# Kernel optimization log

Hardware: AMD Instinct MI355X
Metric: run time of the kernel (lower is better)

The kernel has to match this reference:

```python
import jax, jax.numpy as jnp
import numpy as np

B, NS, D, NE = 4096, 64, 256, 16  # walkers, determinant slots, d_model, electrons


def setup_inputs() -> dict:
    key = jax.random.key(0)
    k_y, k_up, k_dn, k_r = jax.random.split(key, 4)
    y = jax.random.normal(k_y, (B, NS, D), dtype=jnp.float32)
    # xavier_uniform over (d_model, Ne) fan axes
    limit = np.sqrt(6.0 / (D + NE)).astype(np.float32)
    M1_up_real = jax.random.uniform(k_up, (NS, D, NE), dtype=jnp.float32, minval=-limit, maxval=limit)
    M1_down_real = jax.random.uniform(k_dn, (NS, D, NE), dtype=jnp.float32, minval=-limit, maxval=limit)
    # R: Ne distinct orbital-row indices per walker in [0, 2*Ns)
    keys = jax.random.split(k_r, B)
    R = jax.vmap(lambda k: jax.random.permutation(k, 2 * NS)[:NE])(keys).astype(jnp.int32)
    return {"y": y, "M1_up_real": M1_up_real, "M1_down_real": M1_down_real, "R": R}


def reference(y, M1_up_real, M1_down_real, R):
    # orbitals: per-slot linear map of features -> Ne orbital values
    orb_up = jnp.einsum('bnd,nde->bne', y, M1_up_real)      # (B, Ns, Ne)
    orb_dn = jnp.einsum('bnd,nde->bne', y, M1_down_real)    # (B, Ns, Ne)
    orbitals = jnp.concatenate((orb_up, orb_dn), axis=1)     # (B, 2*Ns, Ne)
    # gather Ne rows per walker -> batched square matrices (B, Ne, Ne)
    A = jnp.take_along_axis(orbitals, R[:, :, None], axis=1)
    sign, logabsdet = jnp.linalg.slogdet(A)
    cdtype = jnp.complex64
    amp = logabsdet.astype(cdtype) + jnp.log(sign.astype(cdtype))
    return jnp.where(jnp.isnan(amp), -jnp.inf, amp)          # (B,) complex64
```

## Files before the change

kernel.cpp:

```cpp
#include <hip/hip_runtime.h>
#include <math.h>

#define BWALK 4096
#define NS 64
#define DD 256
#define NE 16
#define NSLOT 128
#define CHUNK 512
#define ROWB 528

typedef __attribute__((ext_vector_type(4))) float f32x4;
typedef __attribute__((ext_vector_type(8))) short s16x8;

union Frag  { s16x8 v; unsigned u[4]; uint4 q; };

__device__ inline unsigned rne_bf16(float x) {
    unsigned u = __float_as_uint(x);
    return (u + 0x7fffu + ((u >> 16) & 1u)) >> 16;
}
__device__ inline float bf16_to_f(unsigned h) { return __uint_as_float(h << 16); }

__global__ __launch_bounds__(256) void convert_m_kernel(
    const float* __restrict__ Mup,
    const float* __restrict__ Mdn,
    uint4* __restrict__ Mhi,
    uint4* __restrict__ Mlo)
{
    const int t = blockIdx.x * 256 + threadIdx.x;
    const int n    = t >> 9;
    const int kc   = (t >> 6) & 7;
    const int lane = t & 63;
    const int kg = lane >> 4;
    const int e  = lane & 15;

    const float* Msrc = (n < NS ? Mup : Mdn) + (size_t)(n & (NS - 1)) * (DD * NE);

    unsigned h[8], l[8];
    #pragma unroll
    for (int j = 0; j < 8; ++j) {
        const int k = kc * 32 + kg * 8 + j;
        const float f = Msrc[k * 16 + e];
        const unsigned hh = rne_bf16(f);
        h[j] = hh;
        l[j] = rne_bf16(f - bf16_to_f(hh));
    }
    uint4 vh, vl;
    vh.x = h[0] | (h[1] << 16); vh.y = h[2] | (h[3] << 16);
    vh.z = h[4] | (h[5] << 16); vh.w = h[6] | (h[7] << 16);
    vl.x = l[0] | (l[1] << 16); vl.y = l[2] | (l[3] << 16);
    vl.z = l[4] | (l[5] << 16); vl.w = l[6] | (l[7] << 16);
    Mhi[t] = vh;
    Mlo[t] = vl;
}

__global__ __launch_bounds__(256) void orbitals_kernel(
    const float* __restrict__ y,
    const int* __restrict__ R,
    const uint4* __restrict__ Mhi,
    const uint4* __restrict__ Mlo,
    float* __restrict__ A)
{
    const int n   = blockIdx.x;
    const int b0  = blockIdx.y * CHUNK;
    const int tid = threadIdx.x;
    const int lane = tid & 63;
    const int wv   = tid >> 6;

    __shared__ __align__(16) unsigned char sY[4 * 2 * 16 * ROWB];
    __shared__ int sCode[CHUNK];
    __shared__ int wsum[4];

    int m[2];
    int cnt = 0;
    #pragma unroll
    for (int q = 0; q < 2; ++q) {
        const int b = b0 + tid * 2 + q;
        const int4* rp = (const int4*)(R + (size_t)b * NE);
        int mi = -1;
        #pragma unroll
        for (int t4 = 0; t4 < 4; ++t4) {
            const int4 r4 = rp[t4];
            if (r4.x == n) mi = t4 * 4 + 0;
            if (r4.y == n) mi = t4 * 4 + 1;
            if (r4.z == n) mi = t4 * 4 + 2;
            if (r4.w == n) mi = t4 * 4 + 3;
        }
        m[q] = mi;
        cnt += (mi >= 0) ? 1 : 0;
    }

    int incl = cnt;
    #pragma unroll
    for (int off = 1; off < 64; off <<= 1) {
        const int x = __shfl_up(incl, off, 64);
        if (lane >= off) incl += x;
    }
    if (lane == 63) wsum[wv] = incl;
    __syncthreads();
    int base = incl - cnt;
    #pragma unroll
    for (int w = 0; w < 3; ++w) if (w < wv) base += wsum[w];
    const int total = wsum[0] + wsum[1] + wsum[2] + wsum[3];
    {
        int p = base;
        #pragma unroll
        for (int q = 0; q < 2; ++q) {
            if (m[q] >= 0) {
                const int b = b0 + tid * 2 + q;
                sCode[p++] = (b << 4) | m[q];
            }
        }
    }
    __syncthreads();

    if (total == 0) return;

    const int e  = lane & 15;
    const int kg = lane >> 4;
    const int slot = n & (NS - 1);
    const uint4* bhp = Mhi + ((size_t)n * 8) * 64 + lane;
    const uint4* blp = Mlo + ((size_t)n * 8) * 64 + lane;

    char* waveBase = (char*)sY + wv * (2 * 16 * ROWB);
    char* hiBase = waveBase;
    char* loBase = waveBase + 16 * ROWB;

    for (int g = wv * 16; g < total; g += 64) {
        Frag BH[8], BL[8];
        #pragma unroll
        for (int kc = 0; kc < 8; ++kc) {
            BH[kc].q = bhp[kc * 64];
            BL[kc].q = blp[kc * 64];
        }

        f32x4 vv[16];
        #pragma unroll
        for (int r = 0; r < 16; ++r) {
            const int idx = g + r;
            const int code = sCode[idx < total ? idx : (total - 1)];
            const float* row = y + ((size_t)(code >> 4) * NS + slot) * DD;
            vv[r] = ((const f32x4*)row)[lane];
        }
        #pragma unroll
        for (int r = 0; r < 16; ++r) {
            unsigned h[4], l[4];
            #pragma unroll
            for (int j = 0; j < 4; ++j) {
                const float f = vv[r][j];
                h[j] = rne_bf16(f);
                l[j] = rne_bf16(f - bf16_to_f(h[j]));
            }
            uint2 hw, lw;
            hw.x = h[0] | (h[1] << 16); hw.y = h[2] | (h[3] << 16);
            lw.x = l[0] | (l[1] << 16); lw.y = l[2] | (l[3] << 16);
            *(uint2*)(hiBase + r * ROWB + lane * 8) = hw;
            *(uint2*)(loBase + r * ROWB + lane * 8) = lw;
        }

        const int gme = g + e;
        const int mycode = sCode[gme < total ? gme : (total - 1)];

        f32x4 acc0 = {0.f, 0.f, 0.f, 0.f};
        f32x4 acc1 = {0.f, 0.f, 0.f, 0.f};
        f32x4 acc2 = {0.f, 0.f, 0.f, 0.f};
        #pragma unroll
        for (int kc = 0; kc < 8; ++kc) {
            Frag ahi, alo;
            ahi.q = *(const uint4*)(hiBase + e * ROWB + kg * 16 + kc * 64);
            alo.q = *(const uint4*)(loBase + e * ROWB + kg * 16 + kc * 64);
            acc0 = __builtin_amdgcn_mfma_f32_16x16x32_bf16(ahi.v, BH[kc].v, acc0, 0, 0, 0);
            acc1 = __builtin_amdgcn_mfma_f32_16x16x32_bf16(ahi.v, BL[kc].v, acc1, 0, 0, 0);
            acc2 = __builtin_amdgcn_mfma_f32_16x16x32_bf16(alo.v, BH[kc].v, acc2, 0, 0, 0);
        }
        const f32x4 acc = acc0 + (acc1 + acc2);

        #pragma unroll
        for (int r = 0; r < 4; ++r) {
            const int j = kg * 4 + r;
            const int jcode = __shfl(mycode, j, 16);
            if (g + j < total) A[(size_t)jcode * NE + e] = acc[r];
        }
    }
}

__global__ __launch_bounds__(256) void lu_det_kernel(
    const float* __restrict__ A, float* __restrict__ out, int mode)
{
    const int tid = threadIdx.x;
    const int w = blockIdx.x * 16 + (tid >> 4);
    const int lane = tid & 15;

    float a[NE];
    {
        const f32x4* p = (const f32x4*)(A + ((size_t)w * NE + lane) * NE);
        #pragma unroll
        for (int q = 0; q < 4; ++q) {
            const f32x4 vv = p[q];
            a[q * 4 + 0] = vv[0]; a[q * 4 + 1] = vv[1];
            a[q * 4 + 2] = vv[2]; a[q * 4 + 3] = vv[3];
        }
    }

    unsigned used = 0u;
    float logabs = 0.0f;
    int neg = 0;
    int perm[NE];

    #pragma unroll
    for (int k = 0; k < NE; ++k) {
        float v = ((used >> lane) & 1u) ? -1.0f : fabsf(a[k]);
        int bi = lane;
        #pragma unroll
        for (int off = 8; off > 0; off >>= 1) {
            const float ov = __shfl_xor(v, off, 16);
            const int   oi = __shfl_xor(bi, off, 16);
            if (ov > v || (ov == v && oi < bi)) { v = ov; bi = oi; }
        }
        const int p = bi;
        perm[k] = p;
        const float pivval = __shfl(a[k], p, 16);
        const bool active = (((used >> lane) & 1u) == 0u) && (lane != p);
        const float mlt = active ? (a[k] / pivval) : 0.0f;
        #pragma unroll
        for (int ee = k + 1; ee < NE; ++ee) {
            const float pe = __shfl(a[ee], p, 16);
            a[ee] = fmaf(-mlt, pe, a[ee]);
        }
        used |= (1u << p);
        logabs += logf(fabsf(pivval));
        neg ^= (pivval < 0.0f) ? 1 : 0;
    }

    int inv = 0;
    #pragma unroll
    for (int k1 = 0; k1 < NE; ++k1) {
        #pragma unroll
        for (int k2 = k1 + 1; k2 < NE; ++k2)
            inv ^= (perm[k1] > perm[k2]) ? 1 : 0;
    }
    neg ^= inv;

    if (lane == 0) {
        float re = logabs;
        float im = neg ? 3.14159274101257324f : 0.0f;
        if (__builtin_isnan(re)) { re = -INFINITY; im = 0.0f; }
        else if (re == -INFINITY) { im = 0.0f; }
        if (mode == 0) { out[2 * w] = re; out[2 * w + 1] = im; }
        else           { out[w] = re; }
    }
}

__global__ __launch_bounds__(256) void outputheaddet_kernel(
    const float* __restrict__ y,
    const float* __restrict__ Mup,
    const float* __restrict__ Mdn,
    const int* __restrict__ R,
    float* __restrict__ out,
    int mode)
{
    const int b = blockIdx.x;
    const int tid = threadIdx.x;

    __shared__ int   sR[NE];
    __shared__ float sYf[NE][DD];
    __shared__ float sA[NE][NE + 1];

    if (tid < NE) sR[tid] = R[b * NE + tid];
    __syncthreads();

    {
        const int i  = tid >> 4;
        const int d0 = (tid & 15) * 16;
        const int n    = sR[i];
        const int slot = n & (NS - 1);
        const float4* yp = reinterpret_cast<const float4*>(
            y + (((size_t)b * NS + slot) * DD + d0));
        float4 v0 = yp[0], v1 = yp[1], v2 = yp[2], v3 = yp[3];
        float4* dst = reinterpret_cast<float4*>(&sYf[i][d0]);
        dst[0] = v0; dst[1] = v1; dst[2] = v2; dst[3] = v3;
    }
    __syncthreads();

    {
        const int i = tid >> 4;
        const int e = tid & 15;
        const int n    = sR[i];
        const int slot = n & (NS - 1);
        const float* Mp = (n < NS ? Mup : Mdn) + (size_t)slot * (DD * NE) + e;
        float acc = 0.0f;
        #pragma unroll 8
        for (int d = 0; d < DD; ++d)
            acc = fmaf(sYf[i][d], Mp[(size_t)d * NE], acc);
        sA[i][e] = acc;
    }
    __syncthreads();

    if (tid >= NE) return;

    const int lane = tid;
    float a[NE];
    #pragma unroll
    for (int e = 0; e < NE; ++e) a[e] = sA[lane][e];

    unsigned used = 0u;
    float logabs = 0.0f;
    int neg = 0;
    int perm[NE];

    #pragma unroll
    for (int k = 0; k < NE; ++k) {
        float v = ((used >> lane) & 1u) ? -1.0f : fabsf(a[k]);
        int bi = lane;
        #pragma unroll
        for (int off = 8; off > 0; off >>= 1) {
            float ov = __shfl_xor(v, off, 16);
            int   oi = __shfl_xor(bi, off, 16);
            if (ov > v || (ov == v && oi < bi)) { v = ov; bi = oi; }
        }
        const int p = bi;
        perm[k] = p;
        const float pivval = __shfl(a[k], p, 16);
        const bool active = (((used >> lane) & 1u) == 0u) && (lane != p);
        const float mlt = active ? (a[k] / pivval) : 0.0f;
        #pragma unroll
        for (int e = k + 1; e < NE; ++e) {
            const float pe = __shfl(a[e], p, 16);
            a[e] = fmaf(-mlt, pe, a[e]);
        }
        used |= (1u << p);
        logabs += logf(fabsf(pivval));
        neg ^= (pivval < 0.0f) ? 1 : 0;
    }

    int inv = 0;
    #pragma unroll
    for (int k1 = 0; k1 < NE; ++k1) {
        #pragma unroll
        for (int k2 = k1 + 1; k2 < NE; ++k2)
            inv ^= (perm[k1] > perm[k2]) ? 1 : 0;
    }
    neg ^= inv;

    if (lane == 0) {
        float re = logabs;
        float im = neg ? 3.14159274101257324f : 0.0f;
        if (__builtin_isnan(re)) { re = -INFINITY; im = 0.0f; }
        else if (re == -INFINITY) { im = 0.0f; }
        if (mode == 0) { out[2 * b] = re; out[2 * b + 1] = im; }
        else           { out[b] = re; }
    }
}

extern "C" void kernel_launch(void* const* d_in, const int* in_sizes, int n_in,
                              void* d_out, int out_size, void* d_ws, size_t ws_size,
                              hipStream_t stream) {
    const float* y   = (const float*)d_in[0];
    const float* Mup = (const float*)d_in[1];
    const float* Mdn = (const float*)d_in[2];
    const int*   R   = (const int*)d_in[3];
    float* out = (float*)d_out;

    const int mode = (out_size >= 2 * BWALK) ? 0 : 1;

    const size_t frag_bytes = (size_t)NSLOT * 8 * 64 * 16;
    const size_t off_Mlo = frag_bytes;
    const size_t off_A   = 2 * frag_bytes;
    const size_t need    = off_A + (size_t)BWALK * NE * NE * sizeof(float);

    if (ws_size >= need) {
        uint4* MhiP = (uint4*)d_ws;
        uint4* MloP = (uint4*)((char*)d_ws + off_Mlo);
        float* A    = (float*)((char*)d_ws + off_A);

        hipLaunchKernelGGL(convert_m_kernel, dim3(NSLOT * 8 * 64 / 256), dim3(256), 0, stream,
                           Mup, Mdn, MhiP, MloP);
        hipLaunchKernelGGL(orbitals_kernel, dim3(NSLOT, BWALK / CHUNK), dim3(256), 0, stream,
                           y, R, MhiP, MloP, A);
        hipLaunchKernelGGL(lu_det_kernel, dim3(BWALK / 16), dim3(256), 0, stream,
                           A, out, mode);
    } else {
        hipLaunchKernelGGL(outputheaddet_kernel, dim3(BWALK), dim3(256), 0, stream,
                           y, Mup, Mdn, R, out, mode);
    }
}
```

Baseline: 41.68 us.

## Fuse M bf16 split conversion into orbitals kernel and halve y staging

Removes the separate conversion kernel: each orbitals block now converts its slot's M weights into hi/lo bf16 fragments in shared memory, and the MFMA loop reads B fragments from LDS instead of global memory. The y row staging is split into two 128-wide halves, which halves the per-wave LDS tile and the registers held in flight. This saves a kernel launch and the workspace round trip, but every block (8 per slot) now redoes the M conversion, and there are extra LDS reads per MFMA step.

```diff
diff --git a/kernel.cpp b/kernel.cpp
--- a/kernel.cpp
+++ b/kernel.cpp
@@ -7,7 +7,7 @@
 #define NE 16
 #define NSLOT 128
 #define CHUNK 512
-#define ROWB 528
+#define ROWBH 264
 
 typedef __attribute__((ext_vector_type(4))) float f32x4;
 typedef __attribute__((ext_vector_type(8))) short s16x8;
@@ -20,44 +20,11 @@
 }
 __device__ inline float bf16_to_f(unsigned h) { return __uint_as_float(h << 16); }
 
-__global__ __launch_bounds__(256) void convert_m_kernel(
+__global__ __launch_bounds__(256) void orbitals_fused_kernel(
+    const float* __restrict__ y,
     const float* __restrict__ Mup,
     const float* __restrict__ Mdn,
-    uint4* __restrict__ Mhi,
-    uint4* __restrict__ Mlo)
-{
-    const int t = blockIdx.x * 256 + threadIdx.x;
-    const int n    = t >> 9;
-    const int kc   = (t >> 6) & 7;
-    const int lane = t & 63;
-    const int kg = lane >> 4;
-    const int e  = lane & 15;
-
-    const float* Msrc = (n < NS ? Mup : Mdn) + (size_t)(n & (NS - 1)) * (DD * NE);
-
-    unsigned h[8], l[8];
-    #pragma unroll
-    for (int j = 0; j < 8; ++j) {
-        const int k = kc * 32 + kg * 8 + j;
-        const float f = Msrc[k * 16 + e];
-        const unsigned hh = rne_bf16(f);
-        h[j] = hh;
-        l[j] = rne_bf16(f - bf16_to_f(hh));
-    }
-    uint4 vh, vl;
-    vh.x = h[0] | (h[1] << 16); vh.y = h[2] | (h[3] << 16);
-    vh.z = h[4] | (h[5] << 16); vh.w = h[6] | (h[7] << 16);
-    vl.x = l[0] | (l[1] << 16); vl.y = l[2] | (l[3] << 16);
-    vl.z = l[4] | (l[5] << 16); vl.w = l[6] | (l[7] << 16);
-    Mhi[t] = vh;
-    Mlo[t] = vl;
-}
-
-__global__ __launch_bounds__(256) void orbitals_kernel(
-    const float* __restrict__ y,
     const int* __restrict__ R,
-    const uint4* __restrict__ Mhi,
-    const uint4* __restrict__ Mlo,
     float* __restrict__ A)
 {
     const int n   = blockIdx.x;
@@ -66,7 +33,9 @@
     const int lane = tid & 63;
     const int wv   = tid >> 6;
 
-    __shared__ __align__(16) unsigned char sY[4 * 2 * 16 * ROWB];
+    __shared__ uint4 sBH[8 * 64];
+    __shared__ uint4 sBL[8 * 64];
+    __shared__ __align__(16) unsigned char sY[4 * 2 * 16 * ROWBH];
     __shared__ int sCode[CHUNK];
     __shared__ int wsum[4];
 
@@ -96,7 +65,35 @@
         if (lane >= off) incl += x;
     }
     if (lane == 63) wsum[wv] = incl;
-    __syncthreads();
+
+    {
+        const float* Msrc = (n < NS ? Mup : Mdn) + (size_t)(n & (NS - 1)) * (DD * NE);
+        #pragma unroll
+        for (int pp = 0; pp < 2; ++pp) {
+            const int p  = tid + pp * 256;
+            const int kc = p >> 6;
+            const int lt = p & 63;
+            const int kg = lt >> 4;
+            const int e  = lt & 15;
+            unsigned h[8], l[8];
+            #pragma unroll
+            for (int j = 0; j < 8; ++j) {
+                const float f = Msrc[(kc * 32 + kg * 8 + j) * 16 + e];
+                const unsigned hh = rne_bf16(f);
+                h[j] = hh;
+                l[j] = rne_bf16(f - bf16_to_f(hh));
+            }
+            uint4 vh, vl;
+            vh.x = h[0] | (h[1] << 16); vh.y = h[2] | (h[3] << 16);
+            vh.z = h[4] | (h[5] << 16); vh.w = h[6] | (h[7] << 16);
+            vl.x = l[0] | (l[1] << 16); vl.y = l[2] | (l[3] << 16);
+            vl.z = l[4] | (l[5] << 16); vl.w = l[6] | (l[7] << 16);
+            sBH[p] = vh;
+            sBL[p] = vl;
+        }
+    }
+    __syncthreads();
+
     int base = incl - cnt;
     #pragma unroll
     for (int w = 0; w < 3; ++w) if (w < wv) base += wsum[w];
@@ -118,59 +115,58 @@
     const int e  = lane & 15;
     const int kg = lane >> 4;
     const int slot = n & (NS - 1);
-    const uint4* bhp = Mhi + ((size_t)n * 8) * 64 + lane;
-    const uint4* blp = Mlo + ((size_t)n * 8) * 64 + lane;
-
-    char* waveBase = (char*)sY + wv * (2 * 16 * ROWB);
+
+    char* waveBase = (char*)sY + wv * (2 * 16 * ROWBH);
     char* hiBase = waveBase;
-    char* loBase = waveBase + 16 * ROWB;
+    char* loBase = waveBase + 16 * ROWBH;
 
     for (int g = wv * 16; g < total; g += 64) {
-        Frag BH[8], BL[8];
-        #pragma unroll
-        for (int kc = 0; kc < 8; ++kc) {
-            BH[kc].q = bhp[kc * 64];
-            BL[kc].q = blp[kc * 64];
-        }
-
-        f32x4 vv[16];
-        #pragma unroll
-        for (int r = 0; r < 16; ++r) {
-            const int idx = g + r;
-            const int code = sCode[idx < total ? idx : (total - 1)];
-            const float* row = y + ((size_t)(code >> 4) * NS + slot) * DD;
-            vv[r] = ((const f32x4*)row)[lane];
-        }
-        #pragma unroll
-        for (int r = 0; r < 16; ++r) {
-            unsigned h[4], l[4];
-            #pragma unroll
-            for (int j = 0; j < 4; ++j) {
-                const float f = vv[r][j];
-                h[j] = rne_bf16(f);
-                l[j] = rne_bf16(f - bf16_to_f(h[j]));
-            }
-            uint2 hw, lw;
-            hw.x = h[0] | (h[1] << 16); hw.y = h[2] | (h[3] << 16);
-            lw.x = l[0] | (l[1] << 16); lw.y = l[2] | (l[3] << 16);
-            *(uint2*)(hiBase + r * ROWB + lane * 8) = hw;
-            *(uint2*)(loBase + r * ROWB + lane * 8) = lw;
-        }
-
         const int gme = g + e;
         const int mycode = sCode[gme < total ? gme : (total - 1)];
 
         f32x4 acc0 = {0.f, 0.f, 0.f, 0.f};
         f32x4 acc1 = {0.f, 0.f, 0.f, 0.f};
         f32x4 acc2 = {0.f, 0.f, 0.f, 0.f};
-        #pragma unroll
-        for (int kc = 0; kc < 8; ++kc) {
-            Frag ahi, alo;
-            ahi.q = *(const uint4*)(hiBase + e * ROWB + kg * 16 + kc * 64);
-            alo.q = *(const uint4*)(loBase + e * ROWB + kg * 16 + kc * 64);
-            acc0 = __builtin_amdgcn_mfma_f32_16x16x32_bf16(ahi.v, BH[kc].v, acc0, 0, 0, 0);
-            acc1 = __builtin_amdgcn_mfma_f32_16x16x32_bf16(ahi.v, BL[kc].v, acc1, 0, 0, 0);
-            acc2 = __builtin_amdgcn_mfma_f32_16x16x32_bf16(alo.v, BH[kc].v, acc2, 0, 0, 0);
+
+        #pragma unroll
+        for (int h = 0; h < 2; ++h) {
+            f32x4 vv[8];
+            #pragma unroll
+            for (int rr = 0; rr < 8; ++rr) {
+                const int idx = g + 2 * rr + (lane >> 5);
+                const int code = sCode[idx < total ? idx : (total - 1)];
+                const float* row = y + ((size_t)(code >> 4) * NS + slot) * DD;
+                vv[rr] = *(const f32x4*)(row + h * 128 + (lane & 31) * 4);
+            }
+            #pragma unroll
+            for (int rr = 0; rr < 8; ++rr) {
+                unsigned hh[4], ll[4];
+                #pragma unroll
+                for (int j = 0; j < 4; ++j) {
+                    const float f = vv[rr][j];
+                    hh[j] = rne_bf16(f);
+                    ll[j] = rne_bf16(f - bf16_to_f(hh[j]));
+                }
+                uint2 hw, lw;
+                hw.x = hh[0] | (hh[1] << 16); hw.y = hh[2] | (hh[3] << 16);
+                lw.x = ll[0] | (ll[1] << 16); lw.y = ll[2] | (ll[3] << 16);
+                const int r = 2 * rr + (lane >> 5);
+                *(uint2*)(hiBase + r * ROWBH + (lane & 31) * 8) = hw;
+                *(uint2*)(loBase + r * ROWBH + (lane & 31) * 8) = lw;
+            }
+
+            #pragma unroll
+            for (int kcl = 0; kcl < 4; ++kcl) {
+                const int kc = h * 4 + kcl;
+                Frag ahi, alo, bh, bl;
+                ahi.q = *(const uint4*)(hiBase + e * ROWBH + kcl * 64 + kg * 16);
+                alo.q = *(const uint4*)(loBase + e * ROWBH + kcl * 64 + kg * 16);
+                bh.q = sBH[kc * 64 + lane];
+                bl.q = sBL[kc * 64 + lane];
+                acc0 = __builtin_amdgcn_mfma_f32_16x16x32_bf16(ahi.v, bh.v, acc0, 0, 0, 0);
+                acc1 = __builtin_amdgcn_mfma_f32_16x16x32_bf16(ahi.v, bl.v, acc1, 0, 0, 0);
+                acc2 = __builtin_amdgcn_mfma_f32_16x16x32_bf16(alo.v, bh.v, acc2, 0, 0, 0);
+            }
         }
         const f32x4 acc = acc0 + (acc1 + acc2);
 
@@ -323,9 +319,9 @@
         const bool active = (((used >> lane) & 1u) == 0u) && (lane != p);
         const float mlt = active ? (a[k] / pivval) : 0.0f;
         #pragma unroll
-        for (int e = k + 1; e < NE; ++e) {
-            const float pe = __shfl(a[e], p, 16);
-            a[e] = fmaf(-mlt, pe, a[e]);
+        for (int e2 = k + 1; e2 < NE; ++e2) {
+            const float pe = __shfl(a[e2], p, 16);
+            a[e2] = fmaf(-mlt, pe, a[e2]);
         }
         used |= (1u << p);
         logabs += logf(fabsf(pivval));
@@ -361,21 +357,12 @@
     float* out = (float*)d_out;
 
     const int mode = (out_size >= 2 * BWALK) ? 0 : 1;
-
-    const size_t frag_bytes = (size_t)NSLOT * 8 * 64 * 16;
-    const size_t off_Mlo = frag_bytes;
-    const size_t off_A   = 2 * frag_bytes;
-    const size_t need    = off_A + (size_t)BWALK * NE * NE * sizeof(float);
-
-    if (ws_size >= need) {
-        uint4* MhiP = (uint4*)d_ws;
-        uint4* MloP = (uint4*)((char*)d_ws + off_Mlo);
-        float* A    = (float*)((char*)d_ws + off_A);
-
-        hipLaunchKernelGGL(convert_m_kernel, dim3(NSLOT * 8 * 64 / 256), dim3(256), 0, stream,
-                           Mup, Mdn, MhiP, MloP);
-        hipLaunchKernelGGL(orbitals_kernel, dim3(NSLOT, BWALK / CHUNK), dim3(256), 0, stream,
-                           y, R, MhiP, MloP, A);
+    const size_t needA = (size_t)BWALK * NE * NE * sizeof(float);
+
+    if (ws_size >= needA) {
+        float* A = (float*)d_ws;
+        hipLaunchKernelGGL(orbitals_fused_kernel, dim3(NSLOT, BWALK / CHUNK), dim3(256), 0, stream,
+                           y, Mup, Mdn, R, A);
         hipLaunchKernelGGL(lu_det_kernel, dim3(BWALK / 16), dim3(256), 0, stream,
                            A, out, mode);
     } else {
```

New measurement: 41.71 us. Within noise of the previous version (+0.1%).
